# Optimization experiments

Measured on AMD Instinct MI355X. Metric: run time of the kernel, lower is better.

Reference implementation:

```python
import jax, jax.numpy as jnp
import numpy as np

NTYPE, NWAVE, NIPS = 4, 8, 3
NUMATOM, NPAIR = 20000, 1000000
CUTOFF = 5.0
NUM_OC = 2
# index_para: angular-block id for each of the 1+3+9=13 angular channels
INDEX_PARA = jnp.array([0] + [1] * 3 + [2] * 9, dtype=jnp.int32)


def setup_inputs() -> dict:
    key = jax.random.key(0)
    ks = jax.random.split(key, 10)
    cart = jax.random.normal(ks[0], (NUMATOM, 3), dtype=jnp.float32) * 3.0
    neigh_list = jax.random.randint(ks[1], (2, NPAIR), 0, NUMATOM)
    shifts = jax.random.normal(ks[2], (NPAIR, 3), dtype=jnp.float32)
    species = jax.random.randint(ks[3], (NUMATOM,), 0, NTYPE)
    rs = jax.random.uniform(ks[4], (NTYPE, NWAVE), dtype=jnp.float32) * CUTOFF
    inta = jax.random.uniform(ks[5], (NTYPE, NWAVE), dtype=jnp.float32) + 0.5
    params = jax.random.normal(ks[6], (NTYPE, NWAVE * NIPS), dtype=jnp.float32)
    hyper = jax.random.normal(ks[7], (NUM_OC + 1, NIPS, NWAVE, NWAVE), dtype=jnp.float32)
    hyper = hyper / jnp.linalg.norm(hyper, axis=2, keepdims=True)  # F.normalize(dim=2)
    D = NWAVE * NIPS
    ocW = jax.random.normal(ks[8], (NUM_OC, D, D), dtype=jnp.float32) / np.sqrt(D)
    ocEmb = jax.random.normal(ks[9], (NUM_OC, NTYPE, D), dtype=jnp.float32)
    return {"cart": cart, "shifts": shifts, "rs": rs, "inta": inta,
            "params": params, "hyper": hyper, "ocW": ocW, "ocEmb": ocEmb,
            "neigh_list": neigh_list, "species": species}


def _forward(cart, shifts, rs, inta, params, hyper, ocW, ocEmb, neigh_list, species):
    numatom = cart.shape[0]
    i_center, j_neigh = neigh_list[0], neigh_list[1]
    neigh_species = species[j_neigh]                       # (P,)
    dvec = cart[i_center] - cart[j_neigh] - shifts         # (P,3)
    dist = jnp.linalg.norm(dvec, axis=-1)                  # (P,)
    u = dvec / dist[:, None]
    # cutoff_cosine
    cut = jnp.square(0.5 * jnp.cos(dist * (np.pi / CUTOFF)) + 0.5)
    # species-gathered Gaussian radial basis (vectorized per-type loop)
    radial = jnp.exp(-inta[neigh_species] * jnp.square(dist[:, None] - rs[neigh_species]))  # (P,nwave)
    # angular: [1, u, u (x) u] -> (P,13)
    ang = jnp.concatenate([jnp.ones((u.shape[0], 1), u.dtype), u,
                           (u[:, :, None] * u[:, None, :]).reshape(-1, 9)], axis=1)
    orbital = ang[:, :, None] * cut[:, None, None] * radial[:, None, :]  # (P,13,nwave)

    def obtain(hyp, orb_coeff):
        # hyp: (NIPS,nwave,nwave); orb_coeff: (numatom, NIPS*nwave)
        ep = orb_coeff.reshape(numatom, NIPS, NWAVE)[j_neigh][:, INDEX_PARA]  # (P,13,nwave)
        ep1 = hyp[INDEX_PARA]                                                 # (13,nwave,nwave)
        w = jnp.einsum('ijk,jkm->ijm', orbital, ep1) * ep                     # (P,13,nwave)
        sw = jax.ops.segment_sum(w, i_center, num_segments=numatom)           # (A,13,nwave)
        pd = jnp.square(sw)
        den = jax.ops.segment_sum(pd.transpose(1, 0, 2), INDEX_PARA,
                                  num_segments=NIPS).transpose(1, 0, 2)       # (A,NIPS,nwave)
        return den.reshape(numatom, -1)

    orb_coeff = params[species]                            # (A, NIPS*nwave)
    density = obtain(hyper[0], orb_coeff)
    for i in range(ocW.shape[0]):
        orb_coeff = jnp.tanh(density @ ocW[i] + ocEmb[i][species]) + orb_coeff
        density = obtain(hyper[i + 1], orb_coeff)
    return density


def reference(cart, shifts, rs, inta, params, hyper, ocW, ocEmb, neigh_list, species):
    return _forward(cart, shifts, rs, inta, params, hyper, ocW, ocEmb, neigh_list, species)
```

## Files before the change

kernel.cpp:

```cpp
#include <hip/hip_runtime.h>
#include <hip/hip_fp16.h>
#include <math.h>

#define NWAVE 8
#define OCD 24
#define CAP 96

struct __align__(16) Rec {
    __half u[4];
    __half cr[8];
    int jn;
    int pad;
};


__global__ __launch_bounds__(256) void scatter_kernel(
    const int* __restrict__ nl, int* __restrict__ cnt, int* __restrict__ perm, int npair) {
    int p = blockIdx.x * 256 + threadIdx.x;
    if (p >= npair) return;
    int i = nl[p];
    int rank = atomicAdd(&cnt[i], 1);
    if (rank < CAP) perm[i * CAP + rank] = p;
}


__global__ __launch_bounds__(256) void build_kernel(
    const int* __restrict__ nl, const float* __restrict__ cart,
    const float* __restrict__ shifts, const int* __restrict__ species,
    const float* __restrict__ rs, const float* __restrict__ inta,
    const int* __restrict__ cnt, const int* __restrict__ perm,
    Rec* __restrict__ rec, int numatom, int npair) {
    int s = blockIdx.x * 256 + threadIdx.x;
    if (s >= numatom * CAP) return;
    int a = s / CAP;
    int r = s - a * CAP;
    int e = cnt[a];
    e = e < CAP ? e : CAP;
    if (r >= e) return;
    int p = perm[s];
    int j = nl[npair + p];
    float sx = shifts[3 * p + 0], sy = shifts[3 * p + 1], sz = shifts[3 * p + 2];
    float dx = cart[3 * a + 0] - cart[3 * j + 0] - sx;
    float dy = cart[3 * a + 1] - cart[3 * j + 1] - sy;
    float dz = cart[3 * a + 2] - cart[3 * j + 2] - sz;
    float dist = sqrtf(dx * dx + dy * dy + dz * dz);
    float inv = 1.0f / dist;
    float c = 0.5f * __cosf(dist * 0.62831853071795864769f) + 0.5f;
    float cut = c * c;
    int sj = species[j];
    Rec rc;
    rc.u[0] = __float2half(dx * inv);
    rc.u[1] = __float2half(dy * inv);
    rc.u[2] = __float2half(dz * inv);
    rc.u[3] = __float2half(0.f);
#pragma unroll
    for (int k = 0; k < 8; ++k) {
        float dd = dist - rs[sj * 8 + k];
        rc.cr[k] = __float2half(cut * __expf(-inta[sj * 8 + k] * dd * dd));
    }
    rc.jn = j;
    rc.pad = 0;
    int4* dst = (int4*)&rec[s];
    const int4* src = (const int4*)&rc;
    dst[0] = src[0];
    dst[1] = src[1];
}


__global__ void init_oc_kernel(const float* __restrict__ params, const int* __restrict__ species,
                               float* __restrict__ oc, int numatom) {
    int idx = blockIdx.x * blockDim.x + threadIdx.x;
    if (idx >= numatom * OCD) return;
    int a = idx / OCD, d = idx - a * OCD;
    oc[idx] = params[species[a] * OCD + d];
}

__global__ void update_kernel(const float* __restrict__ density,
                              const float* __restrict__ W,
                              const float* __restrict__ emb,
                              const int* __restrict__ species,
                              float* __restrict__ oc, int numatom) {
    int idx = blockIdx.x * blockDim.x + threadIdx.x;
    if (idx >= numatom * OCD) return;
    int a = idx / OCD, d = idx - a * OCD;
    const float* dens = density + a * OCD;
    float s = emb[species[a] * OCD + d];
#pragma unroll
    for (int e = 0; e < OCD; ++e) s += dens[e] * W[e * OCD + d];
    oc[idx] = tanhf(s) + oc[idx];
}


__global__ __launch_bounds__(256) void obtain_kernel(
    const Rec* __restrict__ rec, const int* __restrict__ cnt,
    const float* __restrict__ oc, const float* __restrict__ hyp,
    float* __restrict__ density,
    int numatom) {
    int wave = (int)((blockIdx.x * (size_t)blockDim.x + threadIdx.x) >> 6);
    if (wave >= numatom) return;
    int lane = threadIdx.x & 63;
    int m = lane & 7;
    int pp = lane >> 3;

    float hr[3][8];
#pragma unroll
    for (int ip = 0; ip < 3; ++ip)
#pragma unroll
        for (int k = 0; k < 8; ++k) hr[ip][k] = hyp[(ip * 8 + k) * 8 + m];

    float acc[13];
#pragma unroll
    for (int j = 0; j < 13; ++j) acc[j] = 0.f;

    int e = cnt[wave];
    e = e < CAP ? e : CAP;
    const int4* base = (const int4*)(rec + (size_t)wave * CAP);

    int p = pp;
    if (p < e) {
        int4 lo = base[2 * p];
        int4 hi = base[2 * p + 1];
        while (true) {
            int pn = p + 8;
            bool more = pn < e;
            int4 nlo, nhi;
            if (more) {
                nlo = base[2 * pn];
                nhi = base[2 * pn + 1];
            }
            int jn = ((const int*)&hi)[2];
            const float* ocj = oc + jn * OCD;
            float o0 = ocj[m];
            float o1 = ocj[8 + m];
            float o2 = ocj[16 + m];
            const __half* hl = (const __half*)&lo;
            const __half* hh = (const __half*)&hi;
            float ux = __half2float(hl[0]);
            float uy = __half2float(hl[1]);
            float uz = __half2float(hl[2]);
            float cr[8];
#pragma unroll
            for (int k = 0; k < 4; ++k) cr[k] = __half2float(hl[4 + k]);
#pragma unroll
            for (int k = 0; k < 4; ++k) cr[4 + k] = __half2float(hh[k]);
            float rh0 = 0.f, rh1 = 0.f, rh2 = 0.f;
#pragma unroll
            for (int k = 0; k < 8; ++k) {
                rh0 += cr[k] * hr[0][k];
                rh1 += cr[k] * hr[1][k];
                rh2 += cr[k] * hr[2][k];
            }
            float t0 = rh0 * o0;
            float t1 = rh1 * o1;
            float t2 = rh2 * o2;
            acc[0] += t0;
            acc[1] += ux * t1;
            acc[2] += uy * t1;
            acc[3] += uz * t1;
            float vx = ux * t2, vy = uy * t2, vz = uz * t2;
            acc[4] += ux * vx;
            acc[5] += ux * vy;
            acc[6] += ux * vz;
            acc[7] += uy * vx;
            acc[8] += uy * vy;
            acc[9] += uy * vz;
            acc[10] += uz * vx;
            acc[11] += uz * vy;
            acc[12] += uz * vz;
            if (!more) break;
            p = pn;
            lo = nlo;
            hi = nhi;
        }
    }
#pragma unroll
    for (int j = 0; j < 13; ++j) {
        acc[j] += __shfl_xor(acc[j], 8);
        acc[j] += __shfl_xor(acc[j], 16);
        acc[j] += __shfl_xor(acc[j], 32);
    }
    if (pp == 0) {
        float d0 = acc[0] * acc[0];
        float d1 = acc[1] * acc[1] + acc[2] * acc[2] + acc[3] * acc[3];
        float d2 = 0.f;
#pragma unroll
        for (int j = 4; j < 13; ++j) d2 += acc[j] * acc[j];
        density[wave * OCD + m] = d0;
        density[wave * OCD + 8 + m] = d1;
        density[wave * OCD + 16 + m] = d2;
    }
}


extern "C" void kernel_launch(void* const* d_in, const int* in_sizes, int n_in,
                              void* d_out, int out_size, void* d_ws, size_t ws_size,
                              hipStream_t stream) {
    const float* cart = (const float*)d_in[0];
    const float* shifts = (const float*)d_in[1];
    const float* rs = (const float*)d_in[2];
    const float* inta = (const float*)d_in[3];
    const float* params = (const float*)d_in[4];
    const float* hyper = (const float*)d_in[5];
    const float* ocW = (const float*)d_in[6];
    const float* ocEmb = (const float*)d_in[7];
    const int* nl = (const int*)d_in[8];
    const int* species = (const int*)d_in[9];

    int numatom = in_sizes[0] / 3;
    int npair = in_sizes[8] / 2;
    int ntype = in_sizes[2] / NWAVE;

    char* w = (char*)d_ws;
    Rec* rec = (Rec*)w;
    size_t rec_bytes = (size_t)numatom * CAP * sizeof(Rec);
    int* perm = (int*)(w + rec_bytes);
    int* cnt = perm + (size_t)numatom * CAP;
    float* oc = (float*)(cnt + numatom);
    float* density = (float*)d_out;

    const int tb = 256;
    hipMemsetAsync(cnt, 0, numatom * sizeof(int), stream);
    scatter_kernel<<<(npair + tb - 1) / tb, tb, 0, stream>>>(nl, cnt, perm, npair);
    build_kernel<<<(numatom * CAP + tb - 1) / tb, tb, 0, stream>>>(
        nl, cart, shifts, species, rs, inta, cnt, perm, rec, numatom, npair);
    init_oc_kernel<<<(numatom * OCD + tb - 1) / tb, tb, 0, stream>>>(params, species, oc, numatom);

    int obl = (int)(((size_t)numatom * 64 + tb - 1) / tb);
    obtain_kernel<<<obl, tb, 0, stream>>>(rec, cnt, oc, hyper + 0 * 192, density, numatom);
    for (int it = 0; it < 2; ++it) {
        update_kernel<<<(numatom * OCD + tb - 1) / tb, tb, 0, stream>>>(
            density, ocW + (size_t)it * OCD * OCD, ocEmb + (size_t)it * ntype * OCD, species, oc,
            numatom);
        obtain_kernel<<<obl, tb, 0, stream>>>(rec, cnt, oc, hyper + (size_t)(it + 1) * 192,
                                              density, numatom);
    }
}
```

Measured before the change: 274.4 us.

## Replace per-atom fixed-capacity binning with two-level bucketed CSR sort

Replaces the atomic per-atom scatter into fixed 96-slot arrays plus a separate build pass with a two-level binning. The first pass histograms pairs into 128-atom buckets in shared memory and computes the records directly into coarse bucket storage. The second pass sorts each bucket by atom and writes a compact CSR layout with offsets and counts. The obtain kernel now reads the compact records and splits each atom across two waves, combining partial sums through shared memory. The aim is fewer global atomics, no padded slots, and more parallelism per atom, at the cost of an extra copy pass, a serial prefix scan in each block, and a cap on bucket size.

```diff
diff --git a/kernel.cpp b/kernel.cpp
--- a/kernel.cpp
+++ b/kernel.cpp
@@ -4,66 +4,138 @@
 
 #define NWAVE 8
 #define OCD 24
-#define CAP 96
+#define ABITS 7
+#define APB 128
+#define BCAP 7168
+#define NBUCK_MAX 512
+#define PPT 8
 
 struct __align__(16) Rec {
     __half u[4];
     __half cr[8];
     int jn;
-    int pad;
+    int ia;
 };
 
 
-__global__ __launch_bounds__(256) void scatter_kernel(
-    const int* __restrict__ nl, int* __restrict__ cnt, int* __restrict__ perm, int npair) {
-    int p = blockIdx.x * 256 + threadIdx.x;
-    if (p >= npair) return;
-    int i = nl[p];
-    int rank = atomicAdd(&cnt[i], 1);
-    if (rank < CAP) perm[i * CAP + rank] = p;
-}
-
-
-__global__ __launch_bounds__(256) void build_kernel(
+__global__ __launch_bounds__(256) void binA_kernel(
     const int* __restrict__ nl, const float* __restrict__ cart,
     const float* __restrict__ shifts, const int* __restrict__ species,
     const float* __restrict__ rs, const float* __restrict__ inta,
-    const int* __restrict__ cnt, const int* __restrict__ perm,
-    Rec* __restrict__ rec, int numatom, int npair) {
-    int s = blockIdx.x * 256 + threadIdx.x;
-    if (s >= numatom * CAP) return;
-    int a = s / CAP;
-    int r = s - a * CAP;
-    int e = cnt[a];
-    e = e < CAP ? e : CAP;
-    if (r >= e) return;
-    int p = perm[s];
-    int j = nl[npair + p];
-    float sx = shifts[3 * p + 0], sy = shifts[3 * p + 1], sz = shifts[3 * p + 2];
-    float dx = cart[3 * a + 0] - cart[3 * j + 0] - sx;
-    float dy = cart[3 * a + 1] - cart[3 * j + 1] - sy;
-    float dz = cart[3 * a + 2] - cart[3 * j + 2] - sz;
-    float dist = sqrtf(dx * dx + dy * dy + dz * dz);
-    float inv = 1.0f / dist;
-    float c = 0.5f * __cosf(dist * 0.62831853071795864769f) + 0.5f;
-    float cut = c * c;
-    int sj = species[j];
-    Rec rc;
-    rc.u[0] = __float2half(dx * inv);
-    rc.u[1] = __float2half(dy * inv);
-    rc.u[2] = __float2half(dz * inv);
-    rc.u[3] = __float2half(0.f);
-#pragma unroll
-    for (int k = 0; k < 8; ++k) {
-        float dd = dist - rs[sj * 8 + k];
-        rc.cr[k] = __float2half(cut * __expf(-inta[sj * 8 + k] * dd * dd));
-    }
-    rc.jn = j;
-    rc.pad = 0;
-    int4* dst = (int4*)&rec[s];
-    const int4* src = (const int4*)&rc;
-    dst[0] = src[0];
-    dst[1] = src[1];
+    int* __restrict__ bucketCnt, Rec* __restrict__ coarse, int npair, int nbuck) {
+    __shared__ int hist[NBUCK_MAX];
+    __shared__ int cur[NBUCK_MAX];
+    int tid = threadIdx.x;
+    int wgbase = blockIdx.x * (256 * PPT);
+    for (int b = tid; b < nbuck; b += 256) hist[b] = 0;
+    __syncthreads();
+#pragma unroll
+    for (int k = 0; k < PPT; ++k) {
+        int p = wgbase + k * 256 + tid;
+        if (p < npair) atomicAdd(&hist[nl[p] >> ABITS], 1);
+    }
+    __syncthreads();
+    for (int b = tid; b < nbuck; b += 256) {
+        int n = hist[b];
+        cur[b] = n ? atomicAdd(&bucketCnt[b], n) : 0;
+    }
+    __syncthreads();
+#pragma unroll
+    for (int k = 0; k < PPT; ++k) {
+        int p = wgbase + k * 256 + tid;
+        if (p >= npair) continue;
+        int i = nl[p];
+        int b = i >> ABITS;
+        int slot = atomicAdd(&cur[b], 1);
+        if (slot >= BCAP) continue;
+        int j = nl[npair + p];
+        float dx = cart[3 * i + 0] - cart[3 * j + 0] - shifts[3 * p + 0];
+        float dy = cart[3 * i + 1] - cart[3 * j + 1] - shifts[3 * p + 1];
+        float dz = cart[3 * i + 2] - cart[3 * j + 2] - shifts[3 * p + 2];
+        float dist = sqrtf(dx * dx + dy * dy + dz * dz);
+        float inv = 1.0f / dist;
+        float c = 0.5f * __cosf(dist * 0.62831853071795864769f) + 0.5f;
+        float cut = c * c;
+        int sj = species[j];
+        Rec rc;
+        rc.u[0] = __float2half(dx * inv);
+        rc.u[1] = __float2half(dy * inv);
+        rc.u[2] = __float2half(dz * inv);
+        rc.u[3] = __float2half(0.f);
+#pragma unroll
+        for (int kk = 0; kk < 8; ++kk) {
+            float dd = dist - rs[sj * 8 + kk];
+            rc.cr[kk] = __float2half(cut * __expf(-inta[sj * 8 + kk] * dd * dd));
+        }
+        rc.jn = j;
+        rc.ia = i;
+        int4* dst = (int4*)&coarse[(size_t)b * BCAP + slot];
+        const int4* src = (const int4*)&rc;
+        dst[0] = src[0];
+        dst[1] = src[1];
+    }
+}
+
+
+__global__ __launch_bounds__(256) void binB_kernel(
+    const int* __restrict__ bucketCnt, const Rec* __restrict__ coarse,
+    Rec* __restrict__ recs, int* __restrict__ offs, int* __restrict__ cntA,
+    int numatom, int nbuck) {
+    __shared__ int ia[BCAP];
+    __shared__ int hist[APB];
+    __shared__ int pre[APB];
+    __shared__ int scan[NBUCK_MAX];
+    __shared__ int bbase_s;
+    int b = blockIdx.x;
+    int tid = threadIdx.x;
+    for (int x = tid; x < nbuck; x += 256) {
+        int c = bucketCnt[x];
+        scan[x] = c < BCAP ? c : BCAP;
+    }
+    for (int a = tid; a < APB; a += 256) hist[a] = 0;
+    __syncthreads();
+    if (tid == 0) {
+        int s = 0;
+        for (int x = 0; x < b; ++x) s += scan[x];
+        bbase_s = s;
+    }
+    int Cb = bucketCnt[b];
+    Cb = Cb < BCAP ? Cb : BCAP;
+    int aBase = b << ABITS;
+    const int4* cb = (const int4*)(coarse + (size_t)b * BCAP);
+    for (int t = tid; t < Cb; t += 256) {
+        int i = ((const int*)&cb[2 * t + 1])[3];
+        int a = i - aBase;
+        ia[t] = a;
+        atomicAdd(&hist[a], 1);
+    }
+    __syncthreads();
+    if (tid == 0) {
+        int s = 0;
+        for (int a = 0; a < APB; ++a) {
+            pre[a] = s;
+            s += hist[a];
+        }
+    }
+    __syncthreads();
+    int bbase = bbase_s;
+    int wa = numatom - aBase;
+    wa = wa < APB ? wa : APB;
+    for (int a = tid; a < wa; a += 256) {
+        offs[aBase + a] = bbase + pre[a];
+        cntA[aBase + a] = hist[a];
+    }
+    for (int a = tid; a < APB; a += 256) hist[a] = pre[a];
+    __syncthreads();
+    for (int t = tid; t < Cb; t += 256) {
+        int a = ia[t];
+        int slot = atomicAdd(&hist[a], 1);
+        int4 lo = cb[2 * t];
+        int4 hi = cb[2 * t + 1];
+        int4* dst = (int4*)&recs[(size_t)bbase + slot];
+        dst[0] = lo;
+        dst[1] = hi;
+    }
 }
 
 
@@ -76,10 +148,9 @@
 }
 
 __global__ void update_kernel(const float* __restrict__ density,
-                              const float* __restrict__ W,
-                              const float* __restrict__ emb,
-                              const int* __restrict__ species,
-                              float* __restrict__ oc, int numatom) {
+                              const float* __restrict__ W, const float* __restrict__ emb,
+                              const int* __restrict__ species, float* __restrict__ oc,
+                              int numatom) {
     int idx = blockIdx.x * blockDim.x + threadIdx.x;
     if (idx >= numatom * OCD) return;
     int a = idx / OCD, d = idx - a * OCD;
@@ -92,13 +163,16 @@
 
 
 __global__ __launch_bounds__(256) void obtain_kernel(
-    const Rec* __restrict__ rec, const int* __restrict__ cnt,
-    const float* __restrict__ oc, const float* __restrict__ hyp,
-    float* __restrict__ density,
-    int numatom) {
-    int wave = (int)((blockIdx.x * (size_t)blockDim.x + threadIdx.x) >> 6);
-    if (wave >= numatom) return;
-    int lane = threadIdx.x & 63;
+    const Rec* __restrict__ recs, const int* __restrict__ offs,
+    const int* __restrict__ cntA, const float* __restrict__ oc,
+    const float* __restrict__ hyp, float* __restrict__ density, int numatom) {
+    __shared__ float part[2][2][13][8];
+    int tid = threadIdx.x;
+    int warp = tid >> 6;
+    int slot = warp >> 1;
+    int half = warp & 1;
+    int atom = blockIdx.x * 2 + slot;
+    int lane = tid & 63;
     int m = lane & 7;
     int pp = lane >> 3;
 
@@ -112,16 +186,18 @@
 #pragma unroll
     for (int j = 0; j < 13; ++j) acc[j] = 0.f;
 
-    int e = cnt[wave];
-    e = e < CAP ? e : CAP;
-    const int4* base = (const int4*)(rec + (size_t)wave * CAP);
-
-    int p = pp;
+    int s = 0, e = 0;
+    if (atom < numatom) {
+        s = offs[atom];
+        e = s + cntA[atom];
+    }
+    const int4* base = (const int4*)recs;
+    int p = s + half * 8 + pp;
     if (p < e) {
         int4 lo = base[2 * p];
         int4 hi = base[2 * p + 1];
         while (true) {
-            int pn = p + 8;
+            int pn = p + 16;
             bool more = pn < e;
             int4 nlo, nhi;
             if (more) {
@@ -180,14 +256,22 @@
         acc[j] += __shfl_xor(acc[j], 32);
     }
     if (pp == 0) {
-        float d0 = acc[0] * acc[0];
-        float d1 = acc[1] * acc[1] + acc[2] * acc[2] + acc[3] * acc[3];
+#pragma unroll
+        for (int j = 0; j < 13; ++j) part[slot][half][j][m] = acc[j];
+    }
+    __syncthreads();
+    if (half == 0 && pp == 0 && atom < numatom) {
+        float v[13];
+#pragma unroll
+        for (int j = 0; j < 13; ++j) v[j] = part[slot][0][j][m] + part[slot][1][j][m];
+        float d0 = v[0] * v[0];
+        float d1 = v[1] * v[1] + v[2] * v[2] + v[3] * v[3];
         float d2 = 0.f;
 #pragma unroll
-        for (int j = 4; j < 13; ++j) d2 += acc[j] * acc[j];
-        density[wave * OCD + m] = d0;
-        density[wave * OCD + 8 + m] = d1;
-        density[wave * OCD + 16 + m] = d2;
+        for (int j = 4; j < 13; ++j) d2 += v[j] * v[j];
+        density[atom * OCD + m] = d0;
+        density[atom * OCD + 8 + m] = d1;
+        density[atom * OCD + 16 + m] = d2;
     }
 }
 
@@ -209,29 +293,33 @@
     int numatom = in_sizes[0] / 3;
     int npair = in_sizes[8] / 2;
     int ntype = in_sizes[2] / NWAVE;
+    int nbuck = (numatom + APB - 1) >> ABITS;
 
     char* w = (char*)d_ws;
-    Rec* rec = (Rec*)w;
-    size_t rec_bytes = (size_t)numatom * CAP * sizeof(Rec);
-    int* perm = (int*)(w + rec_bytes);
-    int* cnt = perm + (size_t)numatom * CAP;
-    float* oc = (float*)(cnt + numatom);
+    Rec* coarse = (Rec*)w;
+    size_t coarse_bytes = (size_t)nbuck * BCAP * sizeof(Rec);
+    Rec* recs = (Rec*)(w + coarse_bytes);
+    size_t recs_bytes = (size_t)npair * sizeof(Rec);
+    int* bucketCnt = (int*)(w + coarse_bytes + recs_bytes);
+    int* offs = bucketCnt + nbuck;
+    int* cntA = offs + numatom;
+    float* oc = (float*)(cntA + numatom);
     float* density = (float*)d_out;
 
     const int tb = 256;
-    hipMemsetAsync(cnt, 0, numatom * sizeof(int), stream);
-    scatter_kernel<<<(npair + tb - 1) / tb, tb, 0, stream>>>(nl, cnt, perm, npair);
-    build_kernel<<<(numatom * CAP + tb - 1) / tb, tb, 0, stream>>>(
-        nl, cart, shifts, species, rs, inta, cnt, perm, rec, numatom, npair);
+    hipMemsetAsync(bucketCnt, 0, nbuck * sizeof(int), stream);
+    binA_kernel<<<(npair + tb * PPT - 1) / (tb * PPT), tb, 0, stream>>>(
+        nl, cart, shifts, species, rs, inta, bucketCnt, coarse, npair, nbuck);
+    binB_kernel<<<nbuck, tb, 0, stream>>>(bucketCnt, coarse, recs, offs, cntA, numatom, nbuck);
     init_oc_kernel<<<(numatom * OCD + tb - 1) / tb, tb, 0, stream>>>(params, species, oc, numatom);
 
-    int obl = (int)(((size_t)numatom * 64 + tb - 1) / tb);
-    obtain_kernel<<<obl, tb, 0, stream>>>(rec, cnt, oc, hyper + 0 * 192, density, numatom);
+    int obl = (numatom + 1) / 2;
+    obtain_kernel<<<obl, tb, 0, stream>>>(recs, offs, cntA, oc, hyper + 0 * 192, density, numatom);
     for (int it = 0; it < 2; ++it) {
         update_kernel<<<(numatom * OCD + tb - 1) / tb, tb, 0, stream>>>(
             density, ocW + (size_t)it * OCD * OCD, ocEmb + (size_t)it * ntype * OCD, species, oc,
             numatom);
-        obtain_kernel<<<obl, tb, 0, stream>>>(rec, cnt, oc, hyper + (size_t)(it + 1) * 192,
+        obtain_kernel<<<obl, tb, 0, stream>>>(recs, offs, cntA, oc, hyper + (size_t)(it + 1) * 192,
                                               density, numatom);
     }
 }
```

Result: faster. 259.6 us (-5.4%).
